# Kernel tuning notes

Hardware: AMD Instinct MI355X
Metric: run time of the kernel (lower is better)

## Reference

```python
import jax, jax.numpy as jnp
import numpy as np

N = 262144      # number of points
K = 16          # KNN neighbors -> fixed degree CSR
E = N * K
CLASS_DIM = 40


def setup_inputs() -> dict:
    key = jax.random.key(0)
    ks = jax.random.split(key, 12)
    x = jax.random.normal(ks[0], (N, 3), dtype=jnp.float32)
    indptr = (jnp.arange(N + 1, dtype=jnp.int32) * K)
    indices = jax.random.randint(ks[1], (E,), 0, N, dtype=jnp.int32)

    def xavier(k, fan_out, fan_in):
        bound = np.sqrt(6.0 / (fan_in + fan_out)).astype(np.float32)
        return jax.random.uniform(k, (fan_out, fan_in), dtype=jnp.float32,
                                  minval=-bound, maxval=bound)

    return {
        "x": x, "indptr": indptr, "indices": indices,
        "w1": xavier(ks[2], 64, 3),
        "w2": xavier(ks[3], 64, 64),
        "w3": xavier(ks[4], 64, 64),
        "w4": xavier(ks[5], 128, 64),
        "w5": xavier(ks[6], 1024, 192),
        "wf1": xavier(ks[7], 512, 1024),
        "wf2": xavier(ks[8], 256, 512),
        "wf3": xavier(ks[9], CLASS_DIM, 256),
    }


def reference(x, indptr, indices, w1, w2, w3, w4, w5, wf1, wf2, wf3):
    # mlp1, mlp2 (bias-free Linear + ReLU)
    h = jax.nn.relu(x @ w1.T)          # [N, 64]
    h = jax.nn.relu(h @ w2.T)          # [N, 64]

    # GraphMaxPooling: CSR neighbor max (segment-max over gathered rows)
    n = h.shape[0]
    e = indices.shape[0]
    deg = indptr[1:] - indptr[:-1]                                   # [N]
    seg = jnp.repeat(jnp.arange(n, dtype=jnp.int32), deg,
                     total_repeat_length=e)                          # [E]
    x_gm = jax.ops.segment_max(h[indices], seg, num_segments=n,
                               indices_are_sorted=True)              # [N, 64]

    # mlp3, mlp4
    h3 = jax.nn.relu(h @ w3.T)         # [N, 64]
    h4 = jax.nn.relu(h3 @ w4.T)        # [N, 128]

    # concat neighbor-pooled features with point features, mlp5
    hc = jnp.concatenate([x_gm, h4], axis=1)   # [N, 192]
    h5 = jax.nn.relu(hc @ w5.T)                # [N, 1024]

    # global max pool over points -> [1, 1024]
    g = jnp.max(h5, axis=0, keepdims=True)

    # classifier head (dropout in eval mode = identity)
    f = jax.nn.relu(g @ wf1.T)
    f = jax.nn.relu(f @ wf2.T)
    return f @ wf3.T                            # [1, class_dim]
```

## Files before the change

### kernel.cpp

```cpp
#include <hip/hip_runtime.h>
#include <hip/hip_bf16.h>
#include <stdint.h>

typedef unsigned short u16;
typedef __bf16 bf16x8 __attribute__((ext_vector_type(8)));
typedef float  f32x4  __attribute__((ext_vector_type(4)));
typedef u16    u16x8  __attribute__((ext_vector_type(8)));

__device__ __forceinline__ float bf2f(u16 u) {
    return __uint_as_float(((unsigned)u) << 16);
}
__device__ __forceinline__ u16 f2bf(float f) {
    unsigned u = __float_as_uint(f);
    u += 0x7fffu + ((u >> 16) & 1u);
    return (u16)(u >> 16);
}
__device__ __forceinline__ u16x8 maxu16(u16x8 a, u16x8 b) {
    u16x8 r;
    #pragma unroll
    for (int e = 0; e < 8; ++e) r[e] = a[e] > b[e] ? a[e] : b[e];
    return r;
}

#define MFMA16(a, b, c) __builtin_amdgcn_mfma_f32_16x16x32_bf16(a, b, c, 0, 0, 0)

__device__ u16   h2g_buf[262144 * 64];
__device__ u16   gm_buf [262144 * 64];
__device__ u16   w1b[64 * 3];
__device__ u16   w2b[64 * 64];
__device__ u16   w3t[8  * 64 * 8];
__device__ u16   w4t[16 * 64 * 8];
__device__ u16   w5t[64 * 6 * 64 * 8];
__device__ float g_buf[1024];
__device__ float f1_buf[512];
__device__ float f2_buf[256];

__global__ void k0_zero() { g_buf[threadIdx.x] = 0.f; }

__global__ void kcvt(const float* __restrict__ w1f, const float* __restrict__ w2f,
                     const float* __restrict__ w3f, const float* __restrict__ w4f,
                     const float* __restrict__ w5f)
{
    int i = blockIdx.x * 256 + threadIdx.x;
    if (i < 4096) {
        int o = i, e = o & 7, lane = (o >> 3) & 63, f = o >> 9;
        int ss = f & 1, nt = f >> 1;
        int row = nt * 16 + (lane & 15), k = ss * 32 + (lane >> 4) * 8 + e;
        w3t[o] = f2bf(w3f[row * 64 + k]);
    } else if (i < 12288) {
        int o = i - 4096, e = o & 7, lane = (o >> 3) & 63, f = o >> 9;
        int ss = f & 1, nt = f >> 1;
        int row = nt * 16 + (lane & 15), k = ss * 32 + (lane >> 4) * 8 + e;
        w4t[o] = f2bf(w4f[row * 64 + k]);
    }
    else if (i < 12480)  w1b[i - 12288] = f2bf(w1f[i - 12288]);
    else if (i < 16576)  w2b[i - 12480] = f2bf(w2f[i - 12480]);
    else if (i < 213184) {
        int o    = i - 16576;
        int e    = o & 7;
        int lane = (o >> 3) & 63;
        int sg   = o >> 9;
        int s    = sg % 6, c16 = sg / 6;
        w5t[o] = f2bf(w5f[(c16 * 16 + (lane & 15)) * 192 + s * 32 + (lane >> 4) * 8 + e]);
    }
}

__global__ __launch_bounds__(256) void k1_mlp(const float* __restrict__ xf)
{
    __shared__ __align__(16) u16 sw1[64 * 4];
    __shared__ __align__(16) u16 sx [64 * 4];
    __shared__ __align__(16) u16 sw2[64 * 72];
    __shared__ __align__(16) u16 shA[64 * 72];
    __shared__ __align__(16) u16 sh2[64 * 72];

    const int tid = threadIdx.x;
    const int p0  = blockIdx.x * 64;

    #pragma unroll
    for (int c = 0; c < 2; ++c) {
        int ch = c * 256 + tid;
        int row = ch >> 3, j = ch & 7;
        *(u16x8*)&sw2[row * 72 + j * 8] = *(const u16x8*)&w2b[row * 64 + j * 8];
    }
    if (tid < 192) {
        sw1[(tid / 3) * 4 + tid % 3] = w1b[tid];
        sx [(tid / 3) * 4 + tid % 3] = f2bf(xf[p0 * 3 + tid]);
    }
    __syncthreads();

    {
        int m = tid & 63, ng = tid >> 6;
        float x0 = bf2f(sx[m * 4]), x1 = bf2f(sx[m * 4 + 1]), x2 = bf2f(sx[m * 4 + 2]);
        #pragma unroll
        for (int j = 0; j < 16; ++j) {
            int n = ng * 16 + j;
            float s = x0 * bf2f(sw1[n * 4]) + x1 * bf2f(sw1[n * 4 + 1]) + x2 * bf2f(sw1[n * 4 + 2]);
            shA[m * 72 + n] = f2bf(fmaxf(s, 0.f));
        }
    }
    __syncthreads();

    const int lane = tid & 63, w = tid >> 6, q = lane >> 4, l15 = lane & 15;
    const int mrow = 16 * w;

    f32x4 acc2[4];
    #pragma unroll
    for (int nt = 0; nt < 4; ++nt) acc2[nt] = (f32x4){0.f, 0.f, 0.f, 0.f};
    #pragma unroll
    for (int s = 0; s < 2; ++s) {
        bf16x8 a = *(const bf16x8*)&shA[(mrow + l15) * 72 + s * 32 + q * 8];
        #pragma unroll
        for (int nt = 0; nt < 4; ++nt) {
            bf16x8 b = *(const bf16x8*)&sw2[(nt * 16 + l15) * 72 + s * 32 + q * 8];
            acc2[nt] = MFMA16(a, b, acc2[nt]);
        }
    }
    #pragma unroll
    for (int nt = 0; nt < 4; ++nt)
        #pragma unroll
        for (int r = 0; r < 4; ++r) {
            int m = mrow + q * 4 + r;
            sh2[m * 72 + nt * 16 + l15] = f2bf(fmaxf(acc2[nt][r], 0.f));
        }
    __syncthreads();

    {
        int row = tid >> 2, c = (tid & 3) * 16;
        *(u16x8*)&h2g_buf[(size_t)p0 * 64 + tid * 16]     = *(const u16x8*)&sh2[row * 72 + c];
        *(u16x8*)&h2g_buf[(size_t)p0 * 64 + tid * 16 + 8] = *(const u16x8*)&sh2[row * 72 + c + 8];
    }
}

__global__ __launch_bounds__(256) void k2_pool(const int* __restrict__ idx)
{
    const size_t gt = (size_t)blockIdx.x * 256 + threadIdx.x;
    const size_t p  = gt >> 3;
    const int    c  = (threadIdx.x & 7) * 8;

    u16x8 v[16];
    #pragma unroll
    for (int k = 0; k < 16; ++k) {
        int j = idx[p * 16 + k];
        v[k] = *(const u16x8*)&h2g_buf[(size_t)j * 64 + c];
    }
    u16x8 m = v[0];
    #pragma unroll
    for (int k = 1; k < 16; ++k) m = maxu16(m, v[k]);
    *(u16x8*)&gm_buf[p * 64 + c] = m;
}

__global__ __launch_bounds__(512) void k3_fused(int* __restrict__ gout)
{
    __shared__ __align__(16) u16 lds[24576];
    u16* p0  = lds;
    u16* p1  = lds + 8192;
    u16* p2  = lds + 16384;

    const int tid  = threadIdx.x;
    const int lane = tid & 63, w = tid >> 6, q = lane >> 4, l15 = lane & 15;
    const size_t R0 = (size_t)blockIdx.x * 128;

    #pragma unroll
    for (int c = 0; c < 2; ++c) {
        int i = c * 512 + tid, ra = i >> 3, ja = i & 7;
        *(u16x8*)&p0[ra * 64 + ((ja ^ ra) & 7) * 8] =
            *(const u16x8*)&gm_buf[(R0 + ra) * 64 + ja * 8];
        *(u16x8*)&p1[ra * 64 + ((ja ^ ra) & 7) * 8] =
            *(const u16x8*)&h2g_buf[(R0 + ra) * 64 + ja * 8];
    }
    __syncthreads();

    {
        f32x4 a3[4];
        #pragma unroll
        for (int nt = 0; nt < 4; ++nt) a3[nt] = (f32x4){0.f, 0.f, 0.f, 0.f};
        #pragma unroll
        for (int ss = 0; ss < 2; ++ss) {
            int js = ss * 4 + q, r = w * 16 + l15;
            bf16x8 a = *(const bf16x8*)&p1[r * 64 + ((js ^ r) & 7) * 8];
            #pragma unroll
            for (int nt = 0; nt < 4; ++nt) {
                bf16x8 b = *(const bf16x8*)&w3t[(size_t)(nt * 2 + ss) * 512 + lane * 8];
                a3[nt] = MFMA16(a, b, a3[nt]);
            }
        }
        #pragma unroll
        for (int nt = 0; nt < 4; ++nt)
            #pragma unroll
            for (int r = 0; r < 4; ++r) {
                int m = w * 16 + q * 4 + r;
                int n = nt * 16 + l15;
                p2[m * 64 + (((n >> 3) ^ m) & 7) * 8 + (n & 7)] =
                    f2bf(fmaxf(a3[nt][r], 0.f));
            }
    }

    {
        f32x4 a4[8];
        #pragma unroll
        for (int nt = 0; nt < 8; ++nt) a4[nt] = (f32x4){0.f, 0.f, 0.f, 0.f};
        #pragma unroll
        for (int ss = 0; ss < 2; ++ss) {
            int js = ss * 4 + q, r = w * 16 + l15;
            bf16x8 a = *(const bf16x8*)&p2[r * 64 + ((js ^ r) & 7) * 8];
            #pragma unroll
            for (int nt = 0; nt < 8; ++nt) {
                bf16x8 b = *(const bf16x8*)&w4t[(size_t)(nt * 2 + ss) * 512 + lane * 8];
                a4[nt] = MFMA16(a, b, a4[nt]);
            }
        }
        #pragma unroll
        for (int nt = 0; nt < 8; ++nt)
            #pragma unroll
            for (int r = 0; r < 4; ++r) {
                int m  = w * 16 + q * 4 + r;
                int n4 = nt * 16 + l15;
                int j  = (n4 >> 3) & 7;
                u16* dp = (nt < 4) ? p1 : p2;
                dp[m * 64 + ((j ^ m) & 7) * 8 + (n4 & 7)] = f2bf(fmaxf(a4[nt][r], 0.f));
            }
    }
    __syncthreads();

    int zoff = 0;
    #pragma unroll 1
    for (int cg = 0; cg < 4; ++cg) {
        asm volatile("" : "+v"(zoff));
        f32x4 acc[8][2];
        #pragma unroll
        for (int mt = 0; mt < 8; ++mt)
            #pragma unroll
            for (int nt = 0; nt < 2; ++nt) acc[mt][nt] = (f32x4){0.f, 0.f, 0.f, 0.f};
        #pragma unroll
        for (int s = 0; s < 6; ++s) {
            const u16* pa = (s < 2) ? p0 : ((s < 4) ? p1 : p2);
            int j = (s & 1) * 4 + q;
            bf16x8 b[2];
            #pragma unroll
            for (int nt = 0; nt < 2; ++nt)
                b[nt] = *(const bf16x8*)&w5t[(size_t)(((cg * 16 + w * 2 + nt) * 6 + s)) * 512 + lane * 8];
            bf16x8 a[8];
            #pragma unroll
            for (int mt = 0; mt < 8; ++mt) {
                int r = mt * 16 + l15;
                a[mt] = *(const bf16x8*)&pa[r * 64 + ((j ^ r) & 7) * 8 + zoff];
            }
            #pragma unroll
            for (int mt = 0; mt < 8; ++mt)
                #pragma unroll
                for (int nt = 0; nt < 2; ++nt)
                    acc[mt][nt] = MFMA16(a[mt], b[nt], acc[mt][nt]);
        }

        #pragma unroll
        for (int nt = 0; nt < 2; ++nt) {
            float mx = 0.f;
            #pragma unroll
            for (int mt = 0; mt < 8; ++mt)
                #pragma unroll
                for (int e = 0; e < 4; ++e) mx = fmaxf(mx, acc[mt][nt][e]);
            mx = fmaxf(mx, __shfl_xor(mx, 16, 64));
            mx = fmaxf(mx, __shfl_xor(mx, 32, 64));
            if (q == 0)
                atomicMax(&gout[cg * 256 + w * 32 + nt * 16 + l15], __float_as_int(mx));
        }
    }
}

__global__ void k4_f1(const float* __restrict__ wf1)
{
    int r = blockIdx.x, l = threadIdx.x;
    float s = 0.f;
    #pragma unroll
    for (int i = 0; i < 16; ++i) s += wf1[r * 1024 + i * 64 + l] * g_buf[i * 64 + l];
    #pragma unroll
    for (int o = 32; o; o >>= 1) s += __shfl_down(s, o, 64);
    if (!l) f1_buf[r] = fmaxf(s, 0.f);
}
__global__ void k4_f2(const float* __restrict__ wf2)
{
    int r = blockIdx.x, l = threadIdx.x;
    float s = 0.f;
    #pragma unroll
    for (int i = 0; i < 8; ++i) s += wf2[r * 512 + i * 64 + l] * f1_buf[i * 64 + l];
    #pragma unroll
    for (int o = 32; o; o >>= 1) s += __shfl_down(s, o, 64);
    if (!l) f2_buf[r] = fmaxf(s, 0.f);
}
__global__ void k4_out(const float* __restrict__ wf3, float* __restrict__ out)
{
    int r = blockIdx.x, l = threadIdx.x;
    float s = 0.f;
    #pragma unroll
    for (int i = 0; i < 4; ++i) s += wf3[r * 256 + i * 64 + l] * f2_buf[i * 64 + l];
    #pragma unroll
    for (int o = 32; o; o >>= 1) s += __shfl_down(s, o, 64);
    if (!l) out[r] = s;
}

extern "C" void kernel_launch(void* const* d_in, const int* in_sizes, int n_in,
                              void* d_out, int out_size, void* d_ws, size_t ws_size,
                              hipStream_t stream)
{
    (void)in_sizes; (void)n_in; (void)out_size; (void)d_ws; (void)ws_size;
    const float* x   = (const float*)d_in[0];
    const int*   idx = (const int*)d_in[2];
    const float* w1  = (const float*)d_in[3];
    const float* w2  = (const float*)d_in[4];
    const float* w3  = (const float*)d_in[5];
    const float* w4  = (const float*)d_in[6];
    const float* w5  = (const float*)d_in[7];
    const float* wf1 = (const float*)d_in[8];
    const float* wf2 = (const float*)d_in[9];
    const float* wf3 = (const float*)d_in[10];

    float* gptr;
    hipGetSymbolAddress((void**)&gptr, HIP_SYMBOL(g_buf));

    k0_zero <<<1, 1024, 0, stream>>>();
    kcvt    <<<833, 256, 0, stream>>>(w1, w2, w3, w4, w5);
    k1_mlp  <<<262144 / 64, 256, 0, stream>>>(x);
    k2_pool <<<262144 * 8 / 256, 256, 0, stream>>>(idx);
    k3_fused<<<2048, 512, 0, stream>>>((int*)gptr);
    k4_f1   <<<512, 64, 0, stream>>>(wf1);
    k4_f2   <<<256, 64, 0, stream>>>(wf2);
    k4_out  <<<40, 64, 0, stream>>>(wf3, (float*)d_out);
}
```

Baseline: 385.5 us.

## Fuse neighbor max-pool into MLP kernel with warp-specialized producer pipeline

Drops the separate pool kernel and its gm_buf round trip. The fused kernel now runs 1024-thread blocks: 8 producer waves gather the neighbor rows, reduce them with max, and stage the next 128-row tile into double-buffered LDS. Meanwhile 8 consumer waves run mlp3/mlp4/mlp5 and the global max on the current tile. The aim is to overlap the random-gather latency with MFMA compute and save a global write and read of the pooled features. The cost is fewer blocks (256, each doing 8 tiles), more LDS per block, and half the waves idle during each phase, which can reduce occupancy and parallelism.

```diff
diff --git a/kernel.cpp b/kernel.cpp
--- a/kernel.cpp
+++ b/kernel.cpp
@@ -25,7 +25,6 @@
 #define MFMA16(a, b, c) __builtin_amdgcn_mfma_f32_16x16x32_bf16(a, b, c, 0, 0, 0)
 
 __device__ u16   h2g_buf[262144 * 64];
-__device__ u16   gm_buf [262144 * 64];
 __device__ u16   w1b[64 * 3];
 __device__ u16   w2b[64 * 64];
 __device__ u16   w3t[8  * 64 * 8];
@@ -131,139 +130,157 @@
     }
 }
 
-__global__ __launch_bounds__(256) void k2_pool(const int* __restrict__ idx)
-{
-    const size_t gt = (size_t)blockIdx.x * 256 + threadIdx.x;
-    const size_t p  = gt >> 3;
-    const int    c  = (threadIdx.x & 7) * 8;
-
-    u16x8 v[16];
-    #pragma unroll
-    for (int k = 0; k < 16; ++k) {
-        int j = idx[p * 16 + k];
-        v[k] = *(const u16x8*)&h2g_buf[(size_t)j * 64 + c];
-    }
-    u16x8 m = v[0];
-    #pragma unroll
-    for (int k = 1; k < 16; ++k) m = maxu16(m, v[k]);
-    *(u16x8*)&gm_buf[p * 64 + c] = m;
-}
-
-__global__ __launch_bounds__(512) void k3_fused(int* __restrict__ gout)
-{
-    __shared__ __align__(16) u16 lds[24576];
-    u16* p0  = lds;
-    u16* p1  = lds + 8192;
-    u16* p2  = lds + 16384;
+__global__ __launch_bounds__(1024) void k3_fused(const int* __restrict__ idx,
+                                                 int* __restrict__ gout)
+{
+    __shared__ __align__(16) u16 lds[40960];
+    u16* p2 = lds + 32768;
 
     const int tid  = threadIdx.x;
-    const int lane = tid & 63, w = tid >> 6, q = lane >> 4, l15 = lane & 15;
-    const size_t R0 = (size_t)blockIdx.x * 128;
-
-    #pragma unroll
-    for (int c = 0; c < 2; ++c) {
-        int i = c * 512 + tid, ra = i >> 3, ja = i & 7;
-        *(u16x8*)&p0[ra * 64 + ((ja ^ ra) & 7) * 8] =
-            *(const u16x8*)&gm_buf[(R0 + ra) * 64 + ja * 8];
-        *(u16x8*)&p1[ra * 64 + ((ja ^ ra) & 7) * 8] =
-            *(const u16x8*)&h2g_buf[(R0 + ra) * 64 + ja * 8];
+    const int lane = tid & 63, w = tid >> 6;
+    const int q = lane >> 4, l15 = lane & 15;
+    const int T0 = blockIdx.x * 8;
+
+    auto do_half = [&](size_t R1, int h, u16* p0n, u16* p1n) {
+        int pt = (w - 8) * 64 + lane;
+        int tk = h * 512 + pt;
+        int r  = tk >> 3, jc = tk & 7;
+        const int* ip = &idx[(R1 + r) * 16];
+        u16x8 v[8];
+        #pragma unroll
+        for (int k = 0; k < 8; ++k)
+            v[k] = *(const u16x8*)&h2g_buf[(size_t)ip[k] * 64 + jc * 8];
+        u16x8 m = maxu16(maxu16(maxu16(v[0], v[1]), maxu16(v[2], v[3])),
+                         maxu16(maxu16(v[4], v[5]), maxu16(v[6], v[7])));
+        #pragma unroll
+        for (int k = 0; k < 8; ++k)
+            v[k] = *(const u16x8*)&h2g_buf[(size_t)ip[8 + k] * 64 + jc * 8];
+        m = maxu16(m, maxu16(maxu16(maxu16(v[0], v[1]), maxu16(v[2], v[3])),
+                             maxu16(maxu16(v[4], v[5]), maxu16(v[6], v[7]))));
+        *(u16x8*)&p0n[r * 64 + ((jc ^ r) & 7) * 8] = m;
+        *(u16x8*)&p1n[r * 64 + ((jc ^ r) & 7) * 8] =
+            *(const u16x8*)&h2g_buf[(R1 + r) * 64 + jc * 8];
+    };
+
+    if (w >= 8) {
+        size_t Rp = (size_t)T0 * 128;
+        do_half(Rp, 0, lds, lds + 16384);
+        do_half(Rp, 1, lds, lds + 16384);
     }
     __syncthreads();
 
-    {
-        f32x4 a3[4];
-        #pragma unroll
-        for (int nt = 0; nt < 4; ++nt) a3[nt] = (f32x4){0.f, 0.f, 0.f, 0.f};
-        #pragma unroll
-        for (int ss = 0; ss < 2; ++ss) {
-            int js = ss * 4 + q, r = w * 16 + l15;
-            bf16x8 a = *(const bf16x8*)&p1[r * 64 + ((js ^ r) & 7) * 8];
-            #pragma unroll
-            for (int nt = 0; nt < 4; ++nt) {
-                bf16x8 b = *(const bf16x8*)&w3t[(size_t)(nt * 2 + ss) * 512 + lane * 8];
-                a3[nt] = MFMA16(a, b, a3[nt]);
+    #pragma unroll 1
+    for (int t = 0; t < 8; ++t) {
+        const int cur = t & 1;
+        u16* p0c = lds + (cur ? 8192 : 0);
+        u16* p1c = lds + 16384 + (cur ? 8192 : 0);
+        u16* p0n = lds + (cur ? 0 : 8192);
+        u16* p1n = lds + 16384 + (cur ? 0 : 8192);
+        const size_t R1 = (size_t)(T0 + t + 1) * 128;
+
+        if (w < 8) {
+            {
+                f32x4 a3[4];
+                #pragma unroll
+                for (int nt = 0; nt < 4; ++nt) a3[nt] = (f32x4){0.f, 0.f, 0.f, 0.f};
+                #pragma unroll
+                for (int ss = 0; ss < 2; ++ss) {
+                    int js = ss * 4 + q, r = w * 16 + l15;
+                    bf16x8 a = *(const bf16x8*)&p1c[r * 64 + ((js ^ r) & 7) * 8];
+                    #pragma unroll
+                    for (int nt = 0; nt < 4; ++nt) {
+                        bf16x8 b = *(const bf16x8*)&w3t[(size_t)(nt * 2 + ss) * 512 + lane * 8];
+                        a3[nt] = MFMA16(a, b, a3[nt]);
+                    }
+                }
+                #pragma unroll
+                for (int nt = 0; nt < 4; ++nt)
+                    #pragma unroll
+                    for (int r = 0; r < 4; ++r) {
+                        int m = w * 16 + q * 4 + r;
+                        int n = nt * 16 + l15;
+                        p2[m * 64 + (((n >> 3) ^ m) & 7) * 8 + (n & 7)] =
+                            f2bf(fmaxf(a3[nt][r], 0.f));
+                    }
             }
-        }
-        #pragma unroll
-        for (int nt = 0; nt < 4; ++nt)
-            #pragma unroll
-            for (int r = 0; r < 4; ++r) {
-                int m = w * 16 + q * 4 + r;
-                int n = nt * 16 + l15;
-                p2[m * 64 + (((n >> 3) ^ m) & 7) * 8 + (n & 7)] =
-                    f2bf(fmaxf(a3[nt][r], 0.f));
+
+            {
+                f32x4 a4[8];
+                #pragma unroll
+                for (int nt = 0; nt < 8; ++nt) a4[nt] = (f32x4){0.f, 0.f, 0.f, 0.f};
+                #pragma unroll
+                for (int ss = 0; ss < 2; ++ss) {
+                    int js = ss * 4 + q, r = w * 16 + l15;
+                    bf16x8 a = *(const bf16x8*)&p2[r * 64 + ((js ^ r) & 7) * 8];
+                    #pragma unroll
+                    for (int nt = 0; nt < 8; ++nt) {
+                        bf16x8 b = *(const bf16x8*)&w4t[(size_t)(nt * 2 + ss) * 512 + lane * 8];
+                        a4[nt] = MFMA16(a, b, a4[nt]);
+                    }
+                }
+                #pragma unroll
+                for (int nt = 0; nt < 8; ++nt)
+                    #pragma unroll
+                    for (int r = 0; r < 4; ++r) {
+                        int m  = w * 16 + q * 4 + r;
+                        int n4 = nt * 16 + l15;
+                        int j  = (n4 >> 3) & 7;
+                        u16* dp = (nt < 4) ? p1c : p2;
+                        dp[m * 64 + ((j ^ m) & 7) * 8 + (n4 & 7)] = f2bf(fmaxf(a4[nt][r], 0.f));
+                    }
             }
-    }
-
-    {
-        f32x4 a4[8];
-        #pragma unroll
-        for (int nt = 0; nt < 8; ++nt) a4[nt] = (f32x4){0.f, 0.f, 0.f, 0.f};
-        #pragma unroll
-        for (int ss = 0; ss < 2; ++ss) {
-            int js = ss * 4 + q, r = w * 16 + l15;
-            bf16x8 a = *(const bf16x8*)&p2[r * 64 + ((js ^ r) & 7) * 8];
-            #pragma unroll
-            for (int nt = 0; nt < 8; ++nt) {
-                bf16x8 b = *(const bf16x8*)&w4t[(size_t)(nt * 2 + ss) * 512 + lane * 8];
-                a4[nt] = MFMA16(a, b, a4[nt]);
+        } else if (t < 7) {
+            do_half(R1, 0, p0n, p1n);
+        }
+        __syncthreads();
+
+        if (w < 8) {
+            int zoff = 0;
+            #pragma unroll 1
+            for (int cg = 0; cg < 4; ++cg) {
+                asm volatile("" : "+v"(zoff));
+                f32x4 acc[8][2];
+                #pragma unroll
+                for (int mt = 0; mt < 8; ++mt)
+                    #pragma unroll
+                    for (int nt = 0; nt < 2; ++nt) acc[mt][nt] = (f32x4){0.f, 0.f, 0.f, 0.f};
+                #pragma unroll
+                for (int s = 0; s < 6; ++s) {
+                    const u16* pa = (s < 2) ? p0c : ((s < 4) ? p1c : p2);
+                    int j = (s & 1) * 4 + q;
+                    bf16x8 b[2];
+                    #pragma unroll
+                    for (int nt = 0; nt < 2; ++nt)
+                        b[nt] = *(const bf16x8*)&w5t[(size_t)(((cg * 16 + w * 2 + nt) * 6 + s)) * 512 + lane * 8];
+                    bf16x8 a[8];
+                    #pragma unroll
+                    for (int mt = 0; mt < 8; ++mt) {
+                        int r = mt * 16 + l15;
+                        a[mt] = *(const bf16x8*)&pa[r * 64 + ((j ^ r) & 7) * 8 + zoff];
+                    }
+                    #pragma unroll
+                    for (int mt = 0; mt < 8; ++mt)
+                        #pragma unroll
+                        for (int nt = 0; nt < 2; ++nt)
+                            acc[mt][nt] = MFMA16(a[mt], b[nt], acc[mt][nt]);
+                }
+                #pragma unroll
+                for (int nt = 0; nt < 2; ++nt) {
+                    float mx = 0.f;
+                    #pragma unroll
+                    for (int mt = 0; mt < 8; ++mt)
+                        #pragma unroll
+                        for (int e = 0; e < 4; ++e) mx = fmaxf(mx, acc[mt][nt][e]);
+                    mx = fmaxf(mx, __shfl_xor(mx, 16, 64));
+                    mx = fmaxf(mx, __shfl_xor(mx, 32, 64));
+                    if (q == 0)
+                        atomicMax(&gout[cg * 256 + w * 32 + nt * 16 + l15], __float_as_int(mx));
+                }
             }
-        }
-        #pragma unroll
-        for (int nt = 0; nt < 8; ++nt)
-            #pragma unroll
-            for (int r = 0; r < 4; ++r) {
-                int m  = w * 16 + q * 4 + r;
-                int n4 = nt * 16 + l15;
-                int j  = (n4 >> 3) & 7;
-                u16* dp = (nt < 4) ? p1 : p2;
-                dp[m * 64 + ((j ^ m) & 7) * 8 + (n4 & 7)] = f2bf(fmaxf(a4[nt][r], 0.f));
-            }
-    }
-    __syncthreads();
-
-    int zoff = 0;
-    #pragma unroll 1
-    for (int cg = 0; cg < 4; ++cg) {
-        asm volatile("" : "+v"(zoff));
-        f32x4 acc[8][2];
-        #pragma unroll
-        for (int mt = 0; mt < 8; ++mt)
-            #pragma unroll
-            for (int nt = 0; nt < 2; ++nt) acc[mt][nt] = (f32x4){0.f, 0.f, 0.f, 0.f};
-        #pragma unroll
-        for (int s = 0; s < 6; ++s) {
-            const u16* pa = (s < 2) ? p0 : ((s < 4) ? p1 : p2);
-            int j = (s & 1) * 4 + q;
-            bf16x8 b[2];
-            #pragma unroll
-            for (int nt = 0; nt < 2; ++nt)
-                b[nt] = *(const bf16x8*)&w5t[(size_t)(((cg * 16 + w * 2 + nt) * 6 + s)) * 512 + lane * 8];
-            bf16x8 a[8];
-            #pragma unroll
-            for (int mt = 0; mt < 8; ++mt) {
-                int r = mt * 16 + l15;
-                a[mt] = *(const bf16x8*)&pa[r * 64 + ((j ^ r) & 7) * 8 + zoff];
-            }
-            #pragma unroll
-            for (int mt = 0; mt < 8; ++mt)
-                #pragma unroll
-                for (int nt = 0; nt < 2; ++nt)
-                    acc[mt][nt] = MFMA16(a[mt], b[nt], acc[mt][nt]);
-        }
-
-        #pragma unroll
-        for (int nt = 0; nt < 2; ++nt) {
-            float mx = 0.f;
-            #pragma unroll
-            for (int mt = 0; mt < 8; ++mt)
-                #pragma unroll
-                for (int e = 0; e < 4; ++e) mx = fmaxf(mx, acc[mt][nt][e]);
-            mx = fmaxf(mx, __shfl_xor(mx, 16, 64));
-            mx = fmaxf(mx, __shfl_xor(mx, 32, 64));
-            if (q == 0)
-                atomicMax(&gout[cg * 256 + w * 32 + nt * 16 + l15], __float_as_int(mx));
-        }
+        } else if (t < 7) {
+            do_half(R1, 1, p0n, p1n);
+        }
+        __syncthreads();
     }
 }
 
@@ -320,8 +337,7 @@
     k0_zero <<<1, 1024, 0, stream>>>();
     kcvt    <<<833, 256, 0, stream>>>(w1, w2, w3, w4, w5);
     k1_mlp  <<<262144 / 64, 256, 0, stream>>>(x);
-    k2_pool <<<262144 * 8 / 256, 256, 0, stream>>>(idx);
-    k3_fused<<<2048, 512, 0, stream>>>((int*)gptr);
+    k3_fused<<<256, 1024, 0, stream>>>(idx, (int*)gptr);
     k4_f1   <<<512, 64, 0, stream>>>(wf1);
     k4_f2   <<<256, 64, 0, stream>>>(wf2);
     k4_out  <<<40, 64, 0, stream>>>(wf3, (float*)d_out);
```

Measured after the change: 419.8 us. 1.09x slower.
